# Performance work log

Hardware: AMD Instinct MI355X
Metric: run time of the kernel (lower is better)

Reference implementation:

```python
import jax, jax.numpy as jnp
import numpy as np

B, C, L = 4, 16, 1024
U_SELF, U_CROSS, HID = 32, 16, 128
WIDTH = 128
EPS = 1e-5
LN_EPS = 1e-14


def _band_mask(n, w):
    j = jnp.arange(n)
    lo = j - w // 2
    hi = lo + w
    i = j[:, None]
    return (lo <= i) & (i < hi)  # mask[i, j]: query i attends key j


def _layernorm(x, gamma, beta):
    # channel-first LN over dim 1; gamma/beta shape (C, 1)
    mean = jnp.mean(x, 1, keepdims=True)
    var = jnp.mean((x - mean) ** 2, 1, keepdims=True) + LN_EPS
    return (x - mean) / jnp.sqrt(var) * gamma + beta


def _self_attn(x, Wt, Wx, bh, Wa, ba):
    xt = x.transpose(0, 2, 1)                                # (B,L,C)
    q = xt @ Wt                                              # (B,L,U)
    k = xt @ Wx                                              # (B,L,U)
    h = jnp.tanh(q[:, :, None, :] + k[:, None, :, :] + bh)   # (B,L,L,U)
    e = jnp.squeeze(h @ Wa, -1) + ba                         # (B,L,L)
    e = jnp.exp(e - jnp.max(e, -1, keepdims=True))
    e = jnp.where(_band_mask(e.shape[1], WIDTH), e, 0.0)
    a = e / (jnp.sum(e, -1, keepdims=True) + EPS)
    v = a @ xt                                               # (B,L,C)
    return v.transpose(0, 2, 1)


def _ff(x, W1, b1, W2, b2):
    xt = x.transpose(0, 2, 1)
    h = jax.nn.relu(xt @ W1 + b1)
    return (h @ W2 + b2).transpose(0, 2, 1)


def _transformer(x, Wt, Wx, bh, Wa, ba, g1, be1, W1, b1, W2, b2, g2, be2):
    y = _layernorm(x + _self_attn(x, Wt, Wx, bh, Wa, ba), g1, be1)
    return _layernorm(y + _ff(y, W1, b1, W2, b2), g2, be2)


def _cross(y1, y2, Wq, Wk, Wv):
    y1t = y1.transpose(0, 2, 1)
    y2t = y2.transpose(0, 2, 1)
    q = y1t @ Wq
    k = y2t @ Wk
    v = y2t @ Wv                                             # (B,L,Uc)
    e = (q @ k.transpose(0, 2, 1)) * (1.0 / np.float32(np.sqrt(U_CROSS)))
    e = jnp.where(_band_mask(e.shape[-1], WIDTH), e, -jnp.inf)
    a = jax.nn.softmax(e, -1)
    return (a @ v).transpose(0, 2, 1)                        # (B,Uc,L)


def _forward(x1, x2, t1, t2, cw, top):
    y1 = _transformer(x1, *t1)
    y2 = _transformer(x2, *t2)
    g1, be1, W1, b1, W2, b2, g2, be2 = top
    y = _layernorm(y1 + _cross(y1, y2, *cw), g1, be1)
    return _layernorm(y + _ff(y, W1, b1, W2, b2), g2, be2)


def setup_inputs() -> dict:
    key = jax.random.key(0)
    ks = iter(jax.random.split(key, 64))
    u = lambda shape: jax.random.uniform(next(ks), shape, jnp.float32, -0.02, 0.02)
    n = lambda shape: jax.random.normal(next(ks), shape, jnp.float32) * 0.05
    d = {"x1": jax.random.normal(next(ks), (B, C, L), jnp.float32),
         "x2": jax.random.normal(next(ks), (B, C, L), jnp.float32)}
    for p in ("t1", "t2"):
        d[p + "_Wt"] = u((C, U_SELF)); d[p + "_Wx"] = u((C, U_SELF))
        d[p + "_bh"] = jnp.zeros(U_SELF)
        d[p + "_Wa"] = u((U_SELF, 1)); d[p + "_ba"] = jnp.zeros(1)
        d[p + "_g1"] = jnp.ones((C, 1)); d[p + "_be1"] = jnp.zeros((C, 1))
        d[p + "_W1"] = n((C, HID)); d[p + "_b1"] = jnp.zeros(HID)
        d[p + "_W2"] = n((HID, C)); d[p + "_b2"] = jnp.zeros(C)
        d[p + "_g2"] = jnp.ones((C, 1)); d[p + "_be2"] = jnp.zeros((C, 1))
    d["ca_Wq"] = u((C, U_CROSS)); d["ca_Wk"] = u((C, U_CROSS)); d["ca_Wv"] = u((C, U_CROSS))
    d["g1"] = jnp.ones((C, 1)); d["be1"] = jnp.zeros((C, 1))
    d["W1"] = n((C, HID)); d["b1"] = jnp.zeros(HID)
    d["W2"] = n((HID, C)); d["b2"] = jnp.zeros(C)
    d["g2"] = jnp.ones((C, 1)); d["be2"] = jnp.zeros((C, 1))
    return d


def reference(x1, x2, t1_Wt, t1_Wx, t1_bh, t1_Wa, t1_ba, t1_g1, t1_be1, t1_W1, t1_b1, t1_W2, t1_b2, t1_g2, t1_be2, t2_Wt, t2_Wx, t2_bh, t2_Wa, t2_ba, t2_g1, t2_be1, t2_W1, t2_b1, t2_W2, t2_b2, t2_g2, t2_be2, ca_Wq, ca_Wk, ca_Wv, g1, be1, W1, b1, W2, b2, g2, be2):
    t1 = (t1_Wt, t1_Wx, t1_bh, t1_Wa, t1_ba, t1_g1, t1_be1, t1_W1, t1_b1, t1_W2, t1_b2, t1_g2, t1_be2)
    t2 = (t2_Wt, t2_Wx, t2_bh, t2_Wa, t2_ba, t2_g1, t2_be1, t2_W1, t2_b1, t2_W2, t2_b2, t2_g2, t2_be2)
    cw = (ca_Wq, ca_Wk, ca_Wv)
    top = (g1, be1, W1, b1, W2, b2, g2, be2)
    return _forward(x1, x2, t1, t2, cw, top)
```

## Files before the change

kernel.cpp:

```cpp
#include <hip/hip_runtime.h>


#define L_    1024
#define C_    16
#define US_   32
#define HID_  128
#define TI1   8
#define TI2   8
#define K2    2.885390082f

__device__ __forceinline__ float frcp(float x)  { return __builtin_amdgcn_rcpf(x); }
__device__ __forceinline__ float fexp2(float x) { return __builtin_amdgcn_exp2f(x); }

struct BranchP {
  const float *x, *Wt, *Wx, *bh, *Wa, *ba, *g1, *be1, *W1, *b1, *W2, *b2, *g2, *be2;
  float* y;
};

__global__ __launch_bounds__(256) void branch_kernel(BranchP Pa, BranchP Pb) {
  const BranchP P = blockIdx.z ? Pb : Pa;
  const int b   = blockIdx.y;
  const int i0  = blockIdx.x * TI1;
  const int tid = threadIdx.x;
  const int j0  = max(0, i0 - 63);
  const int j1  = min(L_, i0 + TI1 + 64);
  const int Wd  = j1 - j0;

  __shared__ float xs[C_][137];
  __shared__ union {
    struct { float ks[136][33]; float qs[TI1][33]; } a;
    struct { float W1s[C_][129]; float W2s[HID_][17]; float b1s[HID_]; } bb;
  } ovl;
  __shared__ float es[TI1][129];
  __shared__ float ya[TI1][17];
  __shared__ float Wts[C_][US_], Wxs[C_][US_];
  __shared__ float m2was[US_], bhs[US_];
  __shared__ float g1s[C_], be1s[C_], b2s[C_], g2s[C_], be2s[C_];
  __shared__ float bas;

  float w1r[8], w2r[8], b1r = 0.f;
#pragma unroll
  for (int t = 0; t < 8; ++t) { w1r[t] = P.W1[tid + 256 * t]; w2r[t] = P.W2[tid + 256 * t]; }
  if (tid < HID_) b1r = P.b1[tid];

  for (int idx = tid; idx < C_ * US_; idx += 256) {
    int c = idx >> 5, u = idx & 31;
    Wts[c][u] = K2 * P.Wt[idx];
    Wxs[c][u] = K2 * P.Wx[idx];
  }
  if (tid < US_) { m2was[tid] = -2.0f * P.Wa[tid]; bhs[tid] = K2 * P.bh[tid]; }
  if (tid < C_) {
    g1s[tid] = P.g1[tid]; be1s[tid] = P.be1[tid];
    g2s[tid] = P.g2[tid]; be2s[tid] = P.be2[tid];
    b2s[tid] = P.b2[tid];
  }
  if (tid == 0) bas = P.ba[0];
  for (int idx = tid; idx < C_ * Wd; idx += 256) {
    int c = idx / Wd, jj = idx - c * Wd;
    xs[c][jj] = P.x[(b * C_ + c) * L_ + j0 + jj];
  }
  __syncthreads();

  for (int idx = tid; idx < Wd * US_; idx += 256) {
    int j = idx >> 5, u = idx & 31;
    float a = bhs[u];
#pragma unroll
    for (int c = 0; c < C_; ++c) a = fmaf(xs[c][j], Wxs[c][u], a);
    ovl.a.ks[j][u] = a;
  }
  {
    int i = tid >> 5, u = tid & 31;
    float a = 0.f;
#pragma unroll
    for (int c = 0; c < C_; ++c) a = fmaf(xs[c][i0 - j0 + i], Wts[c][u], a);
    ovl.a.qs[i][u] = a;
  }
  __syncthreads();

  const int il   = tid >> 5;
  const int sub  = tid & 31;
  const int ig   = i0 + il;
  const int jlo  = max(0, ig - 63), jhi = min(L_, ig + 65);
  const int nj   = jhi - jlo;
  const int jb   = jlo - j0;
  const int c16  = sub & 15;
  const int half = sub >> 4;

  float inv;
  {
    float xq[US_];
#pragma unroll
    for (int u = 0; u < US_; ++u) xq[u] = ovl.a.qs[il][u];
    float eacc = bas;
#pragma unroll
    for (int u = 0; u < US_; ++u) eacc -= 0.5f * m2was[u];
    float mx = -1e30f;
    for (int jj = sub; jj < nj; jj += 32) {
      const float* kr = ovl.a.ks[jb + jj];
      float acc = eacc;
#pragma unroll
      for (int u = 0; u < US_; ++u) {
        float t = fexp2(xq[u] + kr[u]);
        acc = fmaf(m2was[u], frcp(1.0f + t), acc);
      }
      es[il][jj] = acc;
      mx = fmaxf(mx, acc);
    }
#pragma unroll
    for (int m = 16; m; m >>= 1) mx = fmaxf(mx, __shfl_xor(mx, m));
    float s = 0.f;
    for (int jj = sub; jj < nj; jj += 32) {
      float v = __expf(es[il][jj] - mx);
      es[il][jj] = v; s += v;
    }
#pragma unroll
    for (int m = 16; m; m >>= 1) s += __shfl_xor(s, m);
    inv = frcp(s + 1e-5f);
  }
  __syncthreads();

#pragma unroll
  for (int t = 0; t < 8; ++t) {
    int idx = tid + 256 * t;
    ovl.bb.W1s[idx >> 7][idx & 127] = w1r[t];
  }
#pragma unroll
  for (int t = 0; t < 8; ++t) {
    int idx = tid + 256 * t;
    ovl.bb.W2s[idx >> 4][idx & 15] = w2r[t];
  }
  if (tid < HID_) ovl.bb.b1s[tid] = b1r;
  float yln;
  {
    float v = 0.f;
    for (int jj = half; jj < nj; jj += 2) v = fmaf(es[il][jj], xs[c16][jb + jj], v);
    v += __shfl_xor(v, 16);
    float y0 = xs[c16][ig - j0] + v * inv;
    float s1 = y0, s2 = y0 * y0;
#pragma unroll
    for (int m = 8; m; m >>= 1) { s1 += __shfl_xor(s1, m); s2 += __shfl_xor(s2, m); }
    float mean = s1 * (1.f / 16.f);
    float var  = s2 * (1.f / 16.f) - mean * mean;
    float rstd = rsqrtf(fmaxf(var, 0.f) + 1e-14f);
    yln = (y0 - mean) * rstd * g1s[c16] + be1s[c16];
    if (half == 0) ya[il][c16] = yln;
  }
  __syncthreads();

#pragma unroll
  for (int t = 0; t < 4; ++t) {
    int u = sub + 32 * t;
    float a = ovl.bb.b1s[u];
#pragma unroll
    for (int c = 0; c < C_; ++c) a = fmaf(ya[il][c], ovl.bb.W1s[c][u], a);
    es[il][u] = fmaxf(a, 0.f);
  }
  __syncthreads();

  {
    float o = 0.f;
    int u0 = half * 64;
#pragma unroll
    for (int uu = 0; uu < 64; ++uu) o = fmaf(es[il][u0 + uu], ovl.bb.W2s[u0 + uu][c16], o);
    o += __shfl_xor(o, 16);
    float y0 = yln + o + b2s[c16];
    float s1 = y0, s2 = y0 * y0;
#pragma unroll
    for (int m = 8; m; m >>= 1) { s1 += __shfl_xor(s1, m); s2 += __shfl_xor(s2, m); }
    float mean = s1 * (1.f / 16.f);
    float var  = s2 * (1.f / 16.f) - mean * mean;
    float rstd = rsqrtf(fmaxf(var, 0.f) + 1e-14f);
    if (half == 0)
      P.y[(b * L_ + ig) * C_ + c16] = (y0 - mean) * rstd * g2s[c16] + be2s[c16];
  }
}

__global__ __launch_bounds__(256) void cross_kernel(
    const float* __restrict__ y1g, const float* __restrict__ y2g,
    const float* Wq, const float* Wk, const float* Wv,
    const float* g1, const float* be1, const float* W1, const float* b1,
    const float* W2, const float* b2, const float* g2, const float* be2,
    float* out) {
  const int b   = blockIdx.y;
  const int i0  = blockIdx.x * TI2;
  const int tid = threadIdx.x;
  const int j0  = max(0, i0 - 63);
  const int j1  = min(L_, i0 + TI2 + 64);
  const int Wd  = j1 - j0;

  __shared__ float y1s[TI2][17];
  __shared__ float y2s[136][17];
  __shared__ float Ms[C_][17];
  __shared__ float zs[TI2][17];
  __shared__ float es[TI2][129];
  __shared__ float ya[TI2][17];
  __shared__ float Wqs[C_][C_], Wks[C_][C_], Wvs[C_][C_];
  __shared__ float W1s[C_][129], W2s[HID_][17], b1s[HID_];
  __shared__ float g1s[C_], be1s[C_], b2s[C_], g2s[C_], be2s[C_];

  {
    int c = tid >> 4, u = tid & 15;
    Wqs[c][u] = Wq[tid]; Wks[c][u] = Wk[tid]; Wvs[c][u] = Wv[tid];
  }
  if (tid < TI2 * C_)
    y1s[tid >> 4][tid & 15] = y1g[(b * L_ + i0 + (tid >> 4)) * C_ + (tid & 15)];
  for (int idx = tid; idx < C_ * HID_; idx += 256) {
    W1s[idx >> 7][idx & 127] = W1[idx];
    W2s[idx >> 4][idx & 15]  = W2[idx];
  }
  if (tid < HID_) b1s[tid] = b1[tid];
  if (tid < C_) {
    g1s[tid] = g1[tid]; be1s[tid] = be1[tid];
    g2s[tid] = g2[tid]; be2s[tid] = be2[tid];
    b2s[tid] = b2[tid];
  }
  for (int idx = tid; idx < Wd * C_; idx += 256) {
    int jj = idx >> 4, c = idx & 15;
    y2s[jj][c] = y2g[(b * L_ + j0 + jj) * C_ + c];
  }
  __syncthreads();

  {
    int c1 = tid >> 4, c2 = tid & 15;
    float m = 0.f;
#pragma unroll
    for (int u = 0; u < C_; ++u) m = fmaf(Wqs[c1][u], Wks[c2][u], m);
    Ms[c1][c2] = 0.25f * m;
  }
  __syncthreads();
  if (tid < TI2 * C_) {
    int i = tid >> 4, c = tid & 15;
    float z = 0.f;
#pragma unroll
    for (int cc = 0; cc < C_; ++cc) z = fmaf(y1s[i][cc], Ms[cc][c], z);
    zs[i][c] = z;
  }
  __syncthreads();

  const int il   = tid >> 5;
  const int sub  = tid & 31;
  const int ig   = i0 + il;
  const int jlo  = max(0, ig - 63), jhi = min(L_, ig + 65);
  const int nj   = jhi - jlo;
  const int jb   = jlo - j0;
  const int c16  = sub & 15;
  const int half = sub >> 4;

  float inv;
  {
    float zr[C_];
#pragma unroll
    for (int c = 0; c < C_; ++c) zr[c] = zs[il][c];
    float mx = -1e30f;
    for (int jj = sub; jj < nj; jj += 32) {
      const float* yr = y2s[jb + jj];
      float a = 0.f;
#pragma unroll
      for (int c = 0; c < C_; ++c) a = fmaf(zr[c], yr[c], a);
      es[il][jj] = a;
      mx = fmaxf(mx, a);
    }
#pragma unroll
    for (int m = 16; m; m >>= 1) mx = fmaxf(mx, __shfl_xor(mx, m));
    float s = 0.f;
    for (int jj = sub; jj < nj; jj += 32) {
      float v = __expf(es[il][jj] - mx);
      es[il][jj] = v; s += v;
    }
#pragma unroll
    for (int m = 16; m; m >>= 1) s += __shfl_xor(s, m);
    inv = frcp(s);
  }
  __syncthreads();

  {
    float w = 0.f;
    for (int jj = half; jj < nj; jj += 2) w = fmaf(es[il][jj], y2s[jb + jj][c16], w);
    w += __shfl_xor(w, 16);
    if (half == 0) zs[il][c16] = w * inv;
  }
  __syncthreads();

  float yln;
  {
    float a = 0.f;
#pragma unroll
    for (int c = 0; c < C_; ++c) a = fmaf(zs[il][c], Wvs[c][c16], a);
    float y0 = y1s[il][c16] + a;
    float s1 = y0, s2 = y0 * y0;
#pragma unroll
    for (int m = 8; m; m >>= 1) { s1 += __shfl_xor(s1, m); s2 += __shfl_xor(s2, m); }
    float mean = s1 * (1.f / 16.f);
    float var  = s2 * (1.f / 16.f) - mean * mean;
    float rstd = rsqrtf(fmaxf(var, 0.f) + 1e-14f);
    yln = (y0 - mean) * rstd * g1s[c16] + be1s[c16];
    if (half == 0) ya[il][c16] = yln;
  }
  __syncthreads();

#pragma unroll
  for (int t = 0; t < 4; ++t) {
    int u = sub + 32 * t;
    float a = b1s[u];
#pragma unroll
    for (int c = 0; c < C_; ++c) a = fmaf(ya[il][c], W1s[c][u], a);
    es[il][u] = fmaxf(a, 0.f);
  }
  __syncthreads();

  {
    float o = 0.f;
    int u0 = half * 64;
#pragma unroll
    for (int uu = 0; uu < 64; ++uu) o = fmaf(es[il][u0 + uu], W2s[u0 + uu][c16], o);
    o += __shfl_xor(o, 16);
    float y0 = yln + o + b2s[c16];
    float s1 = y0, s2 = y0 * y0;
#pragma unroll
    for (int m = 8; m; m >>= 1) { s1 += __shfl_xor(s1, m); s2 += __shfl_xor(s2, m); }
    float mean = s1 * (1.f / 16.f);
    float var  = s2 * (1.f / 16.f) - mean * mean;
    float rstd = rsqrtf(fmaxf(var, 0.f) + 1e-14f);
    if (half == 0) zs[il][c16] = (y0 - mean) * rstd * g2s[c16] + be2s[c16];
  }
  __syncthreads();

  if (tid < C_ * TI2) {
    int c = tid >> 3, i = tid & 7;
    out[(b * C_ + c) * L_ + i0 + i] = zs[i][c];
  }
}

extern "C" void kernel_launch(void* const* d_in, const int* in_sizes, int n_in,
                              void* d_out, int out_size, void* d_ws, size_t ws_size,
                              hipStream_t stream) {
  (void)in_sizes; (void)n_in; (void)out_size; (void)ws_size;
  const float* const* in = reinterpret_cast<const float* const*>(d_in);
  float* y1w = reinterpret_cast<float*>(d_ws);
  float* y2w = y1w + 4 * L_ * C_;

  BranchP Pa { in[0],  in[2],  in[3],  in[4],  in[5],  in[6],  in[7],
               in[8],  in[9],  in[10], in[11], in[12], in[13], in[14], y1w };
  BranchP Pb { in[1],  in[15], in[16], in[17], in[18], in[19], in[20],
               in[21], in[22], in[23], in[24], in[25], in[26], in[27], y2w };

  branch_kernel<<<dim3(L_ / TI1, 4, 2), 256, 0, stream>>>(Pa, Pb);
  cross_kernel<<<dim3(L_ / TI2, 4), 256, 0, stream>>>(
      y1w, y2w, in[28], in[29], in[30],
      in[31], in[32], in[33], in[34], in[35], in[36], in[37], in[38],
      reinterpret_cast<float*>(d_out));
}
```

Before: 172.3 us.

## Drop softmax max pass and halve cross-attention query tile

Both softmaxes now skip the max-reduction pass. The log2(e) factor is folded into the weights and fexp2 is applied directly to the logits, so the exp and sum happen in a single loop. This relies on the logits being bounded: the tanh-based scores are bounded, but the cross-attention dot products could in principle overflow. The cross kernel also processes 4 queries per block with 64 threads per query instead of 8 with 32. That doubles the grid and adds an extra shuffle stage to each reduction.

```diff
diff --git a/kernel.cpp b/kernel.cpp
--- a/kernel.cpp
+++ b/kernel.cpp
@@ -6,8 +6,9 @@
 #define US_   32
 #define HID_  128
 #define TI1   8
-#define TI2   8
+#define TI2   4
 #define K2    2.885390082f
+#define L2E   1.442695041f
 
 __device__ __forceinline__ float frcp(float x)  { return __builtin_amdgcn_rcpf(x); }
 __device__ __forceinline__ float fexp2(float x) { return __builtin_amdgcn_exp2f(x); }
@@ -48,7 +49,7 @@
     Wts[c][u] = K2 * P.Wt[idx];
     Wxs[c][u] = K2 * P.Wx[idx];
   }
-  if (tid < US_) { m2was[tid] = -2.0f * P.Wa[tid]; bhs[tid] = K2 * P.bh[tid]; }
+  if (tid < US_) { m2was[tid] = -K2 * P.Wa[tid]; bhs[tid] = K2 * P.bh[tid]; }
   if (tid < C_) {
     g1s[tid] = P.g1[tid]; be1s[tid] = P.be1[tid];
     g2s[tid] = P.g2[tid]; be2s[tid] = P.be2[tid];
@@ -91,10 +92,10 @@
     float xq[US_];
 #pragma unroll
     for (int u = 0; u < US_; ++u) xq[u] = ovl.a.qs[il][u];
-    float eacc = bas;
+    float eacc = L2E * bas;
 #pragma unroll
     for (int u = 0; u < US_; ++u) eacc -= 0.5f * m2was[u];
-    float mx = -1e30f;
+    float s = 0.f;
     for (int jj = sub; jj < nj; jj += 32) {
       const float* kr = ovl.a.ks[jb + jj];
       float acc = eacc;
@@ -103,15 +104,9 @@
         float t = fexp2(xq[u] + kr[u]);
         acc = fmaf(m2was[u], frcp(1.0f + t), acc);
       }
-      es[il][jj] = acc;
-      mx = fmaxf(mx, acc);
-    }
-#pragma unroll
-    for (int m = 16; m; m >>= 1) mx = fmaxf(mx, __shfl_xor(mx, m));
-    float s = 0.f;
-    for (int jj = sub; jj < nj; jj += 32) {
-      float v = __expf(es[il][jj] - mx);
-      es[il][jj] = v; s += v;
+      float v = fexp2(acc);
+      es[il][jj] = v;
+      s += v;
     }
 #pragma unroll
     for (int m = 16; m; m >>= 1) s += __shfl_xor(s, m);
@@ -189,7 +184,7 @@
   const int Wd  = j1 - j0;
 
   __shared__ float y1s[TI2][17];
-  __shared__ float y2s[136][17];
+  __shared__ float y2s[132][17];
   __shared__ float Ms[C_][17];
   __shared__ float zs[TI2][17];
   __shared__ float es[TI2][129];
@@ -225,7 +220,7 @@
     float m = 0.f;
 #pragma unroll
     for (int u = 0; u < C_; ++u) m = fmaf(Wqs[c1][u], Wks[c2][u], m);
-    Ms[c1][c2] = 0.25f * m;
+    Ms[c1][c2] = (0.25f * L2E) * m;
   }
   __syncthreads();
   if (tid < TI2 * C_) {
@@ -237,47 +232,42 @@
   }
   __syncthreads();
 
-  const int il   = tid >> 5;
-  const int sub  = tid & 31;
+  const int il   = tid >> 6;
+  const int sub  = tid & 63;
   const int ig   = i0 + il;
   const int jlo  = max(0, ig - 63), jhi = min(L_, ig + 65);
   const int nj   = jhi - jlo;
   const int jb   = jlo - j0;
   const int c16  = sub & 15;
-  const int half = sub >> 4;
+  const int quad = sub >> 4;
 
   float inv;
   {
     float zr[C_];
 #pragma unroll
     for (int c = 0; c < C_; ++c) zr[c] = zs[il][c];
-    float mx = -1e30f;
-    for (int jj = sub; jj < nj; jj += 32) {
+    float s = 0.f;
+    for (int jj = sub; jj < nj; jj += 64) {
       const float* yr = y2s[jb + jj];
       float a = 0.f;
 #pragma unroll
       for (int c = 0; c < C_; ++c) a = fmaf(zr[c], yr[c], a);
-      es[il][jj] = a;
-      mx = fmaxf(mx, a);
+      float v = fexp2(a);
+      es[il][jj] = v;
+      s += v;
     }
 #pragma unroll
-    for (int m = 16; m; m >>= 1) mx = fmaxf(mx, __shfl_xor(mx, m));
-    float s = 0.f;
-    for (int jj = sub; jj < nj; jj += 32) {
-      float v = __expf(es[il][jj] - mx);
-      es[il][jj] = v; s += v;
-    }
-#pragma unroll
-    for (int m = 16; m; m >>= 1) s += __shfl_xor(s, m);
+    for (int m = 32; m; m >>= 1) s += __shfl_xor(s, m);
     inv = frcp(s);
   }
   __syncthreads();
 
   {
     float w = 0.f;
-    for (int jj = half; jj < nj; jj += 2) w = fmaf(es[il][jj], y2s[jb + jj][c16], w);
+    for (int jj = quad; jj < nj; jj += 4) w = fmaf(es[il][jj], y2s[jb + jj][c16], w);
     w += __shfl_xor(w, 16);
-    if (half == 0) zs[il][c16] = w * inv;
+    w += __shfl_xor(w, 32);
+    if (quad == 0) zs[il][c16] = w * inv;
   }
   __syncthreads();
 
@@ -294,13 +284,13 @@
     float var  = s2 * (1.f / 16.f) - mean * mean;
     float rstd = rsqrtf(fmaxf(var, 0.f) + 1e-14f);
     yln = (y0 - mean) * rstd * g1s[c16] + be1s[c16];
-    if (half == 0) ya[il][c16] = yln;
-  }
-  __syncthreads();
-
-#pragma unroll
-  for (int t = 0; t < 4; ++t) {
-    int u = sub + 32 * t;
+    if (quad == 0) ya[il][c16] = yln;
+  }
+  __syncthreads();
+
+#pragma unroll
+  for (int t = 0; t < 2; ++t) {
+    int u = sub + 64 * t;
     float a = b1s[u];
 #pragma unroll
     for (int c = 0; c < C_; ++c) a = fmaf(ya[il][c], W1s[c][u], a);
@@ -310,10 +300,11 @@
 
   {
     float o = 0.f;
-    int u0 = half * 64;
-#pragma unroll
-    for (int uu = 0; uu < 64; ++uu) o = fmaf(es[il][u0 + uu], W2s[u0 + uu][c16], o);
+    int u0 = quad * 32;
+#pragma unroll
+    for (int uu = 0; uu < 32; ++uu) o = fmaf(es[il][u0 + uu], W2s[u0 + uu][c16], o);
     o += __shfl_xor(o, 16);
+    o += __shfl_xor(o, 32);
     float y0 = yln + o + b2s[c16];
     float s1 = y0, s2 = y0 * y0;
 #pragma unroll
@@ -321,12 +312,12 @@
     float mean = s1 * (1.f / 16.f);
     float var  = s2 * (1.f / 16.f) - mean * mean;
     float rstd = rsqrtf(fmaxf(var, 0.f) + 1e-14f);
-    if (half == 0) zs[il][c16] = (y0 - mean) * rstd * g2s[c16] + be2s[c16];
+    if (quad == 0) zs[il][c16] = (y0 - mean) * rstd * g2s[c16] + be2s[c16];
   }
   __syncthreads();
 
   if (tid < C_ * TI2) {
-    int c = tid >> 3, i = tid & 7;
+    int c = tid >> 2, i = tid & 3;
     out[(b * C_ + c) * L_ + i0 + i] = zs[i][c];
   }
 }
```

Result: no change. 169.6 us (-1.5%).
